# Performance work log

Hardware: AMD Instinct MI355X
Metric: run time of the kernel (lower is better)

## Reference

```python
import jax, jax.numpy as jnp
import numpy as np

B = 2048          # graphs in dense batch
NPG = 64          # nodes per graph (molecules are small)
N = B * NPG       # 131072 total nodes
E = 524288        # directed edges, avg degree 4
D = 275           # dim_inner
L = 5             # layers_mp
NF = 9            # atom categorical features
V = 128           # per-feature vocab
BN_EPS = 1e-5


def setup_inputs() -> dict:
    key = jax.random.key(0)
    ks = jax.random.split(key, 8)
    return {
        "x_atoms": jax.random.randint(ks[0], (N, NF), 0, 119, dtype=jnp.int64),
        "edge_index": jax.random.randint(ks[1], (2, E), 0, N, dtype=jnp.int64),
        "atom_emb": jax.random.normal(ks[2], (NF, V, D), jnp.float32) * 0.1,
        "conv_W": jax.random.normal(ks[3], (L, D, D), jnp.float32) * (1.0 / np.sqrt(D)),
        "conv_b": jnp.zeros((L, D), jnp.float32),
        "bn_gamma": jnp.ones((L, D), jnp.float32),
        "bn_beta": jnp.zeros((L, D), jnp.float32),
        "post_W": jax.random.normal(ks[4], (D, D), jnp.float32) * (1.0 / np.sqrt(D)),
        "post_b": jnp.zeros((D,), jnp.float32),
    }


def reference(x_atoms, edge_index, atom_emb, conv_W, conv_b, bn_gamma, bn_beta, post_W, post_b):
    n = x_atoms.shape[0]
    # AtomEncoder: sum of per-feature embedding lookups -> [N, D]
    h = jax.vmap(lambda tab, idx: tab[idx], in_axes=(0, 1))(atom_emb, x_atoms).sum(0)

    # GCN normalization with self loops (shared across layers since graph is fixed)
    loops = jnp.arange(n, dtype=edge_index.dtype)
    row = jnp.concatenate([edge_index[0], loops])  # source
    col = jnp.concatenate([edge_index[1], loops])  # target (aggregation index)
    deg = jax.ops.segment_sum(jnp.ones_like(row, h.dtype), col, num_segments=n)
    dinv = jnp.where(deg > 0, jax.lax.rsqrt(jnp.maximum(deg, 1e-12)), 0.0)
    norm = dinv[row] * dinv[col]  # [E+N]

    for i in range(L):
        xw = h @ conv_W[i].T                                   # [N, D] linear (no bias yet)
        msg = norm[:, None] * xw[row]                          # gather + edge scaling
        agg = jax.ops.segment_sum(msg, col, num_segments=n) + conv_b[i]
        # BatchNorm1d (training-mode batch stats, biased variance)
        mu = agg.mean(axis=0)
        var = agg.var(axis=0)
        hbn = (agg - mu) * jax.lax.rsqrt(var + BN_EPS) * bn_gamma[i] + bn_beta[i]
        h = jax.nn.relu(hbn)

    # post_mp: single Linear (MLPNoAct, num_layers=1)
    h = h @ post_W.T + post_b

    # graph_preprocess -> dense batch [B, NPG, D], then pairwise dot-product decode
    hd = h.reshape(B, NPG, D)
    logits = jnp.einsum('bnd,bmd->bnm', hd, hd)[..., None]     # [B, NPG, NPG, 1]
    return logits
```

## Files before the change

### kernel.cpp

```cpp
#include <hip/hip_runtime.h>
#include <hip/hip_bf16.h>
#include <cstdint>

#define NN 131072
#define NE 524288
#define DIM 275
#define DP 288
#define NFEAT 9
#define NVOC 128
#define NLAY 5
#define NPG 64
#define NGRAPH 2048
#define BN_EPS 1e-5f
#define BK 32
#define NEPAD (NE + 3 * NN)
#define LDSE 1536

typedef unsigned short u16;
typedef __attribute__((ext_vector_type(8))) short s16x8;
typedef __attribute__((ext_vector_type(4))) float f32x4;

__device__ __forceinline__ float bf2f(u16 u) {
  union { unsigned int i; float f; } x; x.i = ((unsigned int)u) << 16; return x.f;
}
__device__ __forceinline__ u16 f2bf(float f) {
  union { float f; unsigned int i; } x; x.f = f;
  unsigned int r = x.i + 0x7fffu + ((x.i >> 16) & 1u);
  return (u16)(r >> 16);
}
__device__ __forceinline__ void acc4(float* a, uint2 m) {
  a[0] += bf2f((u16)m.x); a[1] += bf2f((u16)(m.x >> 16));
  a[2] += bf2f((u16)m.y); a[3] += bf2f((u16)(m.y >> 16));
}


__global__ void hist_kernel(const int* __restrict__ ei, int* __restrict__ cnt) {
  int e = blockIdx.x * 256 + threadIdx.x;
  if (e < NE) atomicAdd(&cnt[ei[NE + e]], 1);
}

__global__ void pad_dinv_kernel(const int* __restrict__ cnt, int* __restrict__ cnt_pad,
                                float* __restrict__ dinv) {
  int v = blockIdx.x * 256 + threadIdx.x;
  if (v < NN) {
    int c = cnt[v];
    cnt_pad[v] = (c + 3) & ~3;
    dinv[v] = rsqrtf(1.0f + (float)c);
  }
}

__global__ void scan_block_kernel(const int* __restrict__ in, int* __restrict__ out_ex,
                                  int* __restrict__ partials) {
  __shared__ int buf[2][1024];
  int t = threadIdx.x;
  int idx = blockIdx.x * 1024 + t;
  int v = in[idx];
  buf[0][t] = v;
  __syncthreads();
  int cur = 0;
  for (int off = 1; off < 1024; off <<= 1) {
    int x = buf[cur][t];
    if (t >= off) x += buf[cur][t - off];
    buf[cur ^ 1][t] = x;
    __syncthreads();
    cur ^= 1;
  }
  out_ex[idx] = buf[cur][t] - v;
  if (t == 1023) partials[blockIdx.x] = buf[cur][t];
}

__global__ void scan_partials_kernel(int* partials) {
  __shared__ int buf[2][128];
  int t = threadIdx.x;
  int v = partials[t];
  buf[0][t] = v;
  __syncthreads();
  int cur = 0;
  for (int off = 1; off < 128; off <<= 1) {
    int x = buf[cur][t];
    if (t >= off) x += buf[cur][t - off];
    buf[cur ^ 1][t] = x;
    __syncthreads();
    cur ^= 1;
  }
  partials[t] = buf[cur][t] - v;
}

__global__ void add_offsets_kernel(int* __restrict__ indptr, const int* __restrict__ partials,
                                   int* __restrict__ cursor, const int* __restrict__ cnt_pad) {
  int i = blockIdx.x * 256 + threadIdx.x;
  if (i < NN) {
    int v = indptr[i] + partials[i >> 10];
    indptr[i] = v;
    cursor[i] = v;
    if (i == NN - 1) indptr[NN] = v + cnt_pad[NN - 1];
  }
}

__global__ void fill_csr_kernel(const int* __restrict__ ei, int* __restrict__ cursor,
                                int* __restrict__ srcs) {
  int e = blockIdx.x * 256 + threadIdx.x;
  if (e < NE) {
    int c = ei[NE + e];
    int p = atomicAdd(&cursor[c], 1);
    srcs[p] = ei[e];
  }
}

__global__ void pad_fill_kernel(const int* __restrict__ cursor, const int* __restrict__ indptr,
                                int* __restrict__ srcs) {
  int v = blockIdx.x * 256 + threadIdx.x;
  if (v < NN) {
    int pe = indptr[v + 1];
    for (int p = cursor[v]; p < pe; ++p) srcs[p] = NN;
  }
}

__global__ void zrow_kernel(u16* __restrict__ P, u16* __restrict__ Q) {
  int i = threadIdx.x;
  if (i < DP) {
    P[(size_t)NN * DP + i] = 0;
    Q[(size_t)NN * DP + i] = 0;
  }
}

__global__ void wpad_kernel(const float* __restrict__ convW, const float* __restrict__ postW,
                            u16* __restrict__ Wp) {
  int i = blockIdx.x * 256 + threadIdx.x;
  const int total = 6 * 320 * DP;
  if (i >= total) return;
  int k = i % DP;
  int r = i / DP;
  int j = r % 320;
  int m = r / 320;
  float val = 0.f;
  if (j < DIM && k < DIM)
    val = (m < 5) ? convW[((size_t)m * DIM + j) * DIM + k] : postW[(size_t)j * DIM + k];
  Wp[i] = f2bf(val);
}


__global__ void embed_kernel(const int* __restrict__ xa, const float* __restrict__ emb,
                             u16* __restrict__ P) {
  int n = blockIdx.x;
  int idx[NFEAT];
#pragma unroll
  for (int f = 0; f < NFEAT; ++f) idx[f] = xa[n * NFEAT + f];
  for (int d = threadIdx.x; d < DP; d += 128) {
    float s = 0.f;
    if (d < DIM) {
#pragma unroll
      for (int f = 0; f < NFEAT; ++f) s += emb[((size_t)f * NVOC + idx[f]) * DIM + d];
    }
    P[(size_t)n * DP + d] = f2bf(s);
  }
}


__device__ __forceinline__ uint4 xform8s(uint4 r, const float* __restrict__ sc,
                                         const float* __restrict__ sh, int k) {
  union { uint4 u; u16 h[8]; } in, out;
  in.u = r;
#pragma unroll
  for (int j = 0; j < 8; ++j) {
    float x = fmaf(bf2f(in.h[j]), sc[k + j], sh[k + j]);
    out.h[j] = f2bf(fmaxf(x, 0.f));
  }
  return out.u;
}

__launch_bounds__(256)
__global__ void gemm_kernel(const u16* __restrict__ A, const u16* __restrict__ Wp,
                            u16* __restrict__ C,
                            const float* __restrict__ bn_sum, const float* __restrict__ bn_sq,
                            const float* __restrict__ gamma, const float* __restrict__ beta,
                            const float* __restrict__ rowscale, const float* __restrict__ colbias) {
  __shared__ __align__(16) u16 Asl[64 * BK];
  __shared__ __align__(16) u16 Bsl[288 * BK];
  __shared__ float scs[DP], shs[DP];
  const int tid = threadIdx.x, lane = tid & 63, wv = tid >> 6;
  const int wm = wv & 1, wn = wv >> 1;
  const int row0 = blockIdx.x * 64;
  const bool bn = (bn_sum != nullptr);

  for (int d = tid; d < DP; d += 256) {
    float sc = 1.f, sh = 0.f;
    if (bn) {
      if (d < DIM) {
        const float invN = 1.0f / (float)NN;
        float mu = bn_sum[d] * invN;
        float var = bn_sq[d] * invN - mu * mu;
        float rstd = rsqrtf(var + BN_EPS);
        sc = gamma[d] * rstd;
        sh = fmaf(-mu, sc, beta[d]);
      } else {
        sc = 0.f; sh = 0.f;
      }
    }
    scs[d] = sc; shs[d] = sh;
  }

  const int srow = tid >> 2, schk = tid & 3;
  const int swz = ((schk ^ (srow & 3) ^ ((srow >> 2) & 3)) << 3);
  const int awoff = srow * BK + swz;
  const u16* ag = A + (size_t)(row0 + srow) * DP + schk * 8;
  const u16* bg = Wp + (size_t)srow * DP + schk * 8;
  const bool st4 = (tid < 128);

  const int fr = lane & 15, fs = lane >> 4;
  int aoff[2], boff[9];
#pragma unroll
  for (int i = 0; i < 2; ++i) {
    int r = wm * 32 + i * 16 + fr;
    aoff[i] = r * BK + ((fs ^ (r & 3) ^ ((r >> 2) & 3)) << 3);
  }
#pragma unroll
  for (int j = 0; j < 9; ++j) {
    int r = wn * 144 + j * 16 + fr;
    boff[j] = r * BK + ((fs ^ (r & 3) ^ ((r >> 2) & 3)) << 3);
  }

  uint4 ra = *(const uint4*)(ag);
  uint4 rb0 = *(const uint4*)(bg);
  uint4 rb1 = *(const uint4*)(bg + (size_t)64 * DP);
  uint4 rb2 = *(const uint4*)(bg + (size_t)128 * DP);
  uint4 rb3 = *(const uint4*)(bg + (size_t)192 * DP);
  uint4 rb4;
  if (st4) rb4 = *(const uint4*)(bg + (size_t)256 * DP);
  __syncthreads();
  if (bn) ra = xform8s(ra, scs, shs, schk * 8);
  *(uint4*)&Asl[awoff] = ra;
  *(uint4*)&Bsl[awoff] = rb0;
  *(uint4*)&Bsl[awoff + 64 * BK] = rb1;
  *(uint4*)&Bsl[awoff + 128 * BK] = rb2;
  *(uint4*)&Bsl[awoff + 192 * BK] = rb3;
  if (st4) *(uint4*)&Bsl[awoff + 256 * BK] = rb4;
  __syncthreads();

  f32x4 acc0[9], acc1[9];
#pragma unroll
  for (int j = 0; j < 9; ++j) {
    acc0[j] = (f32x4){0.f, 0.f, 0.f, 0.f};
    acc1[j] = (f32x4){0.f, 0.f, 0.f, 0.f};
  }

#pragma unroll 1
  for (int s = 0; s < 9; ++s) {
    const bool more = (s < 8);
    uint4 na, nb0, nb1, nb2, nb3, nb4;
    if (more) {
      int k = (s + 1) * BK;
      na = *(const uint4*)(ag + k);
      nb0 = *(const uint4*)(bg + k);
      nb1 = *(const uint4*)(bg + (size_t)64 * DP + k);
      nb2 = *(const uint4*)(bg + (size_t)128 * DP + k);
      nb3 = *(const uint4*)(bg + (size_t)192 * DP + k);
      if (st4) nb4 = *(const uint4*)(bg + (size_t)256 * DP + k);
    }
    s16x8 af0 = *(const s16x8*)&Asl[aoff[0]];
    s16x8 af1 = *(const s16x8*)&Asl[aoff[1]];
#pragma unroll
    for (int j = 0; j < 9; ++j) {
      s16x8 bf = *(const s16x8*)&Bsl[boff[j]];
      acc0[j] = __builtin_amdgcn_mfma_f32_16x16x32_bf16(af0, bf, acc0[j], 0, 0, 0);
      acc1[j] = __builtin_amdgcn_mfma_f32_16x16x32_bf16(af1, bf, acc1[j], 0, 0, 0);
    }
    __syncthreads();
    if (more) {
      if (bn) na = xform8s(na, scs, shs, (s + 1) * BK + schk * 8);
      *(uint4*)&Asl[awoff] = na;
      *(uint4*)&Bsl[awoff] = nb0;
      *(uint4*)&Bsl[awoff + 64 * BK] = nb1;
      *(uint4*)&Bsl[awoff + 128 * BK] = nb2;
      *(uint4*)&Bsl[awoff + 192 * BK] = nb3;
      if (st4) *(uint4*)&Bsl[awoff + 256 * BK] = nb4;
      __syncthreads();
    }
  }

#pragma unroll
  for (int i = 0; i < 2; ++i) {
    int gr0 = row0 + wm * 32 + i * 16 + fs * 4;
    float rs[4];
#pragma unroll
    for (int r = 0; r < 4; ++r) rs[r] = rowscale ? rowscale[gr0 + r] : 1.f;
#pragma unroll
    for (int j = 0; j < 9; ++j) {
      f32x4 av = i ? acc1[j] : acc0[j];
      int gc = wn * 144 + j * 16 + fr;
      float cb = (colbias && gc < DIM) ? colbias[gc] : 0.f;
#pragma unroll
      for (int r = 0; r < 4; ++r) {
        u16 o = (gc < DIM) ? f2bf(fmaf(av[r], rs[r], cb)) : (u16)0;
        C[(size_t)(gr0 + r) * DP + gc] = o;
      }
    }
  }
}


__launch_bounds__(256)
__global__ void spmm_kernel(const u16* __restrict__ X, u16* __restrict__ Y,
                            const int* __restrict__ indptr, const int* __restrict__ srcs,
                            const float* __restrict__ dinv, const float* __restrict__ bias,
                            float* __restrict__ bn_sum, float* __restrict__ bn_sq) {
  __shared__ float ls[DP], lq[DP];
  __shared__ int sptr[65];
  __shared__ int sidx[LDSE];
  int tid = threadIdx.x;
  for (int i = tid; i < DP; i += 256) { ls[i] = 0.f; lq[i] = 0.f; }
  int vb = blockIdx.x * 64;
  if (tid < 65) sptr[tid] = indptr[vb + tid];
  __syncthreads();
  int ebase = sptr[0];
  int ecnt = sptr[64] - ebase;
  const int* ip;
  if (ecnt <= LDSE) {
    for (int i = tid; i < ecnt; i += 256) sidx[i] = srcs[ebase + i];
    ip = sidx;
  } else {
    ip = srcs + ebase;
  }
  __syncthreads();

  int lane = tid & 63, wv = tid >> 6;
  int c0 = lane << 2;
  int c1 = 256 + (lane << 2);
  bool tl = lane < 8;
  float bia[4], bib[4];
#pragma unroll
  for (int j = 0; j < 4; ++j) bia[j] = bias[c0 + j];
#pragma unroll
  for (int j = 0; j < 4; ++j) bib[j] = (tl && c1 + j < DIM) ? bias[c1 + j] : 0.f;
  float s0[4] = {}, q0[4] = {}, s1[4] = {}, q1[4] = {};

  for (int g = 0; g < 8; ++g) {
    int nA = wv * 16 + g;
    int nB = nA + 8;
    int ebA = sptr[nA] - ebase, neA = sptr[nA + 1] - sptr[nA];
    int ebB = sptr[nB] - ebase, neB = sptr[nB + 1] - sptr[nB];
    int nemax = neA > neB ? neA : neB;
    const u16* xA = X + (size_t)(vb + nA) * DP;
    const u16* xB = X + (size_t)(vb + nB) * DP;
    uint2 mA = *(const uint2*)(xA + c0);
    uint2 mB = *(const uint2*)(xB + c0);
    uint2 tA, tB;
    if (tl) { tA = *(const uint2*)(xA + c1); tB = *(const uint2*)(xB + c1); }
    float A0[4] = {}, B0[4] = {}, A1[4] = {}, B1[4] = {};
    acc4(A0, mA); acc4(B0, mB);
    if (tl) { acc4(A1, tA); acc4(B1, tB); }

    for (int e = 0; e < nemax; e += 4) {
      bool aA = e < neA, aB = e < neB;
      int oA = aA ? ebA + e : 0;
      int oB = aB ? ebB + e : 0;
      int ia[4], ib[4];
#pragma unroll
      for (int j = 0; j < 4; ++j) {
        int va = ip[oA + j], vbx = ip[oB + j];
        ia[j] = aA ? va : NN;
        ib[j] = aB ? vbx : NN;
      }
      const u16* pa[4]; const u16* pb[4];
#pragma unroll
      for (int j = 0; j < 4; ++j) {
        pa[j] = X + (size_t)ia[j] * DP;
        pb[j] = X + (size_t)ib[j] * DP;
      }
      uint2 ma[4], mb[4];
#pragma unroll
      for (int j = 0; j < 4; ++j) ma[j] = *(const uint2*)(pa[j] + c0);
#pragma unroll
      for (int j = 0; j < 4; ++j) mb[j] = *(const uint2*)(pb[j] + c0);
      uint2 ta[4], tb[4];
      if (tl) {
#pragma unroll
        for (int j = 0; j < 4; ++j) ta[j] = *(const uint2*)(pa[j] + c1);
#pragma unroll
        for (int j = 0; j < 4; ++j) tb[j] = *(const uint2*)(pb[j] + c1);
      }
#pragma unroll
      for (int j = 0; j < 4; ++j) { acc4(A0, ma[j]); acc4(B0, mb[j]); }
      if (tl) {
#pragma unroll
        for (int j = 0; j < 4; ++j) { acc4(A1, ta[j]); acc4(B1, tb[j]); }
      }
    }

    float dvA = dinv[vb + nA], dvB = dinv[vb + nB];
    u16* yA = Y + (size_t)(vb + nA) * DP;
    u16* yB = Y + (size_t)(vb + nB) * DP;
    float ya[4], yb[4];
#pragma unroll
    for (int j = 0; j < 4; ++j) {
      ya[j] = fmaf(dvA, A0[j], bia[j]);
      s0[j] += ya[j]; q0[j] += ya[j] * ya[j];
      yb[j] = fmaf(dvB, B0[j], bia[j]);
      s0[j] += yb[j]; q0[j] += yb[j] * yb[j];
    }
    uint2 wa, wb;
    wa.x = (unsigned)f2bf(ya[0]) | ((unsigned)f2bf(ya[1]) << 16);
    wa.y = (unsigned)f2bf(ya[2]) | ((unsigned)f2bf(ya[3]) << 16);
    wb.x = (unsigned)f2bf(yb[0]) | ((unsigned)f2bf(yb[1]) << 16);
    wb.y = (unsigned)f2bf(yb[2]) | ((unsigned)f2bf(yb[3]) << 16);
    *(uint2*)(yA + c0) = wa;
    *(uint2*)(yB + c0) = wb;
    if (tl) {
      float za[4], zb[4];
#pragma unroll
      for (int j = 0; j < 4; ++j) {
        za[j] = fmaf(dvA, A1[j], bib[j]);
        s1[j] += za[j]; q1[j] += za[j] * za[j];
        zb[j] = fmaf(dvB, B1[j], bib[j]);
        s1[j] += zb[j]; q1[j] += zb[j] * zb[j];
      }
      uint2 ua, ub;
      ua.x = (unsigned)f2bf(za[0]) | ((unsigned)f2bf(za[1]) << 16);
      ua.y = (unsigned)f2bf(za[2]) | ((unsigned)f2bf(za[3]) << 16);
      ub.x = (unsigned)f2bf(zb[0]) | ((unsigned)f2bf(zb[1]) << 16);
      ub.y = (unsigned)f2bf(zb[2]) | ((unsigned)f2bf(zb[3]) << 16);
      *(uint2*)(yA + c1) = ua;
      *(uint2*)(yB + c1) = ub;
    }
  }

#pragma unroll
  for (int j = 0; j < 4; ++j) { atomicAdd(&ls[c0 + j], s0[j]); atomicAdd(&lq[c0 + j], q0[j]); }
  if (tl) {
#pragma unroll
    for (int j = 0; j < 4; ++j) { atomicAdd(&ls[c1 + j], s1[j]); atomicAdd(&lq[c1 + j], q1[j]); }
  }
  __syncthreads();
  for (int i = tid; i < DP; i += 256) {
    atomicAdd(&bn_sum[i], ls[i]);
    atomicAdd(&bn_sq[i], lq[i]);
  }
}


__launch_bounds__(256)
__global__ void decode_kernel(const u16* __restrict__ H, float* __restrict__ out) {
  __shared__ __align__(16) u16 tile[4][2][NPG * BK];
  int tid = threadIdx.x, lane = tid & 63, wv = tid >> 6;
  int g = blockIdx.x * 4 + wv;
  const u16* Hg = H + (size_t)g * NPG * DP;
  const int ssl = lane & 3;
  int soff[4];
  const u16* sg[4];
#pragma unroll
  for (int i = 0; i < 4; ++i) {
    int r = (lane >> 2) + i * 16;
    soff[i] = r * BK + ((ssl ^ (r & 3) ^ ((r >> 2) & 3)) << 3);
    sg[i] = Hg + (size_t)r * DP + ssl * 8;
  }
  const int fr = lane & 15, fs = lane >> 4;
  const int fswz = ((fs ^ (fr & 3) ^ ((fr >> 2) & 3)) << 3);
  int foff[4];
#pragma unroll
  for (int i = 0; i < 4; ++i) foff[i] = (i * 16 + fr) * BK + fswz;

  u16* t0 = tile[wv][0];
  u16* t1 = tile[wv][1];
  uint4 rg[4];
#pragma unroll
  for (int i = 0; i < 4; ++i) rg[i] = *(const uint4*)(sg[i]);
#pragma unroll
  for (int i = 0; i < 4; ++i) *(uint4*)&t0[soff[i]] = rg[i];

  f32x4 acc[4][4];
#pragma unroll
  for (int i = 0; i < 4; ++i)
#pragma unroll
    for (int j = 0; j < 4; ++j) acc[i][j] = (f32x4){0.f, 0.f, 0.f, 0.f};

  for (int s = 0; s < DP / BK; ++s) {
    u16* cur = (s & 1) ? t1 : t0;
    u16* nxt = (s & 1) ? t0 : t1;
    const bool more = (s < DP / BK - 1);
    if (more) {
#pragma unroll
      for (int i = 0; i < 4; ++i) rg[i] = *(const uint4*)(sg[i] + (s + 1) * BK);
    }
    s16x8 af[4];
#pragma unroll
    for (int i = 0; i < 4; ++i) af[i] = *(const s16x8*)&cur[foff[i]];
#pragma unroll
    for (int i = 0; i < 4; ++i)
#pragma unroll
      for (int j = 0; j < 4; ++j)
        acc[i][j] = __builtin_amdgcn_mfma_f32_16x16x32_bf16(af[i], af[j], acc[i][j], 0, 0, 0);
    if (more) {
#pragma unroll
      for (int i = 0; i < 4; ++i) *(uint4*)&nxt[soff[i]] = rg[i];
    }
  }
  float* og = out + (size_t)g * NPG * NPG;
#pragma unroll
  for (int i = 0; i < 4; ++i) {
    int m0 = i * 16 + fs * 4;
#pragma unroll
    for (int j = 0; j < 4; ++j) {
      int n = j * 16 + fr;
#pragma unroll
      for (int r = 0; r < 4; ++r) og[(m0 + r) * NPG + n] = acc[i][j][r];
    }
  }
}


extern "C" void kernel_launch(void* const* d_in, const int* in_sizes, int n_in,
                              void* d_out, int out_size, void* d_ws, size_t ws_size,
                              hipStream_t stream) {
  const int* xa = (const int*)d_in[0];
  const int* ei = (const int*)d_in[1];
  const float* emb = (const float*)d_in[2];
  const float* convW = (const float*)d_in[3];
  const float* convB = (const float*)d_in[4];
  const float* gamma = (const float*)d_in[5];
  const float* beta = (const float*)d_in[6];
  const float* postW = (const float*)d_in[7];
  const float* postB = (const float*)d_in[8];
  float* out = (float*)d_out;

  char* w = (char*)d_ws;
  u16* P = (u16*)w;          w += (size_t)(NN + 1) * DP * sizeof(u16);
  u16* Q = (u16*)w;          w += (size_t)(NN + 1) * DP * sizeof(u16);
  u16* Wp = (u16*)w;         w += (size_t)6 * 320 * DP * sizeof(u16);
  float* dinv = (float*)w;   w += (size_t)NN * sizeof(float);
  int* cnt = (int*)w;        w += (size_t)NN * sizeof(int);
  int* cnt_pad = (int*)w;    w += (size_t)NN * sizeof(int);
  int* indptr = (int*)w;     w += (size_t)(NN + 64) * sizeof(int);
  int* cursor = (int*)w;     w += (size_t)NN * sizeof(int);
  int* srcs = (int*)w;       w += (size_t)NEPAD * sizeof(int);
  int* partials = (int*)w;   w += 256 * sizeof(int);
  float* bnstats = (float*)w; w += (size_t)NLAY * 2 * DP * sizeof(float);

  size_t need = (size_t)(w - (char*)d_ws);
  if (ws_size < need) return;

  hipMemsetAsync(cnt, 0, (size_t)NN * sizeof(int), stream);
  hipMemsetAsync(bnstats, 0, (size_t)NLAY * 2 * DP * sizeof(float), stream);
  hist_kernel<<<NE / 256, 256, 0, stream>>>(ei, cnt);
  pad_dinv_kernel<<<NN / 256, 256, 0, stream>>>(cnt, cnt_pad, dinv);
  scan_block_kernel<<<NN / 1024, 1024, 0, stream>>>(cnt_pad, indptr, partials);
  scan_partials_kernel<<<1, 128, 0, stream>>>(partials);
  add_offsets_kernel<<<NN / 256, 256, 0, stream>>>(indptr, partials, cursor, cnt_pad);
  fill_csr_kernel<<<NE / 256, 256, 0, stream>>>(ei, cursor, srcs);
  pad_fill_kernel<<<NN / 256, 256, 0, stream>>>(cursor, indptr, srcs);
  wpad_kernel<<<(6 * 320 * DP + 255) / 256, 256, 0, stream>>>(convW, postW, Wp);
  embed_kernel<<<NN, 128, 0, stream>>>(xa, emb, P);
  zrow_kernel<<<1, 288, 0, stream>>>(P, Q);

  for (int l = 0; l < NLAY; ++l) {
    const float* bs = l ? bnstats + (size_t)(l - 1) * 2 * DP : nullptr;
    gemm_kernel<<<NN / 64, 256, 0, stream>>>(
        P, Wp + (size_t)l * 320 * DP, Q,
        bs, bs ? bs + DP : nullptr,
        l ? gamma + (size_t)(l - 1) * DIM : nullptr,
        l ? beta + (size_t)(l - 1) * DIM : nullptr,
        dinv, nullptr);
    spmm_kernel<<<NN / 64, 256, 0, stream>>>(Q, P, indptr, srcs, dinv,
                                             convB + (size_t)l * DIM,
                                             bnstats + (size_t)l * 2 * DP,
                                             bnstats + (size_t)l * 2 * DP + DP);
  }

  const float* bs5 = bnstats + (size_t)4 * 2 * DP;
  gemm_kernel<<<NN / 64, 256, 0, stream>>>(
      P, Wp + (size_t)5 * 320 * DP, Q, bs5, bs5 + DP,
      gamma + (size_t)4 * DIM, beta + (size_t)4 * DIM, nullptr, postB);

  decode_kernel<<<NGRAPH / 4, 256, 0, stream>>>(Q, out);
}
```

Before: 1.030 ms.

## Double-buffer GEMM LDS with direct global-to-LDS weight loads; rebalance SpMM tail lanes

The weight matrix is now stored pre-swizzled so the GEMM can copy B tiles straight from global memory into LDS with global_load_lds. A and B tiles are double-buffered, which drops one barrier per k-step and overlaps the next tile's load with the MFMAs. In the SpMM, the 19-column tail of each node pair is spread over 16 lanes (8 per node) instead of 8 lanes each handling both nodes, and edge indices are read from LDS as int4 vectors. The cost is double the GEMM LDS footprint, which may lower occupancy, and int4 index reads that depend on 16-byte-aligned offsets in the padded edge list.

```diff
diff --git a/kernel.cpp b/kernel.cpp
--- a/kernel.cpp
+++ b/kernel.cpp
@@ -20,6 +20,10 @@
 typedef __attribute__((ext_vector_type(8))) short s16x8;
 typedef __attribute__((ext_vector_type(4))) float f32x4;
 
+#define GLL16(g, l) __builtin_amdgcn_global_load_lds( \
+    (const __attribute__((address_space(1))) unsigned int*)(g), \
+    (__attribute__((address_space(3))) unsigned int*)(l), 16, 0, 0)
+
 __device__ __forceinline__ float bf2f(u16 u) {
   union { unsigned int i; float f; } x; x.i = ((unsigned int)u) << 16; return x.f;
 }
@@ -136,7 +140,9 @@
   float val = 0.f;
   if (j < DIM && k < DIM)
     val = (m < 5) ? convW[((size_t)m * DIM + j) * DIM + k] : postW[(size_t)j * DIM + k];
-  Wp[i] = f2bf(val);
+  int s = (j & 3) ^ ((j >> 2) & 3);
+  int kout = (k & ~24) | (((((k >> 3) & 3)) ^ s) << 3);
+  Wp[(size_t)r * DP + kout] = f2bf(val);
 }
 
 
@@ -170,13 +176,13 @@
 }
 
 __launch_bounds__(256)
-__global__ void gemm_kernel(const u16* __restrict__ A, const u16* __restrict__ Wp,
+__global__ void gemm_kernel(const u16* __restrict__ A, const u16* __restrict__ Wq,
                             u16* __restrict__ C,
                             const float* __restrict__ bn_sum, const float* __restrict__ bn_sq,
                             const float* __restrict__ gamma, const float* __restrict__ beta,
                             const float* __restrict__ rowscale, const float* __restrict__ colbias) {
-  __shared__ __align__(16) u16 Asl[64 * BK];
-  __shared__ __align__(16) u16 Bsl[288 * BK];
+  __shared__ __align__(16) u16 Asl[2][64 * BK];
+  __shared__ __align__(16) u16 Bsl[2][288 * BK];
   __shared__ float scs[DP], shs[DP];
   const int tid = threadIdx.x, lane = tid & 63, wv = tid >> 6;
   const int wm = wv & 1, wn = wv >> 1;
@@ -204,8 +210,7 @@
   const int swz = ((schk ^ (srow & 3) ^ ((srow >> 2) & 3)) << 3);
   const int awoff = srow * BK + swz;
   const u16* ag = A + (size_t)(row0 + srow) * DP + schk * 8;
-  const u16* bg = Wp + (size_t)srow * DP + schk * 8;
-  const bool st4 = (tid < 128);
+  const int grow = lane >> 2, gchk = (lane & 3) * 8;
 
   const int fr = lane & 15, fs = lane >> 4;
   int aoff[2], boff[9];
@@ -220,21 +225,12 @@
     boff[j] = r * BK + ((fs ^ (r & 3) ^ ((r >> 2) & 3)) << 3);
   }
 
+  for (int i = wv; i < 18; i += 4)
+    GLL16(Wq + (size_t)(i * 16 + grow) * DP + gchk, &Bsl[0][i * 512]);
   uint4 ra = *(const uint4*)(ag);
-  uint4 rb0 = *(const uint4*)(bg);
-  uint4 rb1 = *(const uint4*)(bg + (size_t)64 * DP);
-  uint4 rb2 = *(const uint4*)(bg + (size_t)128 * DP);
-  uint4 rb3 = *(const uint4*)(bg + (size_t)192 * DP);
-  uint4 rb4;
-  if (st4) rb4 = *(const uint4*)(bg + (size_t)256 * DP);
   __syncthreads();
   if (bn) ra = xform8s(ra, scs, shs, schk * 8);
-  *(uint4*)&Asl[awoff] = ra;
-  *(uint4*)&Bsl[awoff] = rb0;
-  *(uint4*)&Bsl[awoff + 64 * BK] = rb1;
-  *(uint4*)&Bsl[awoff + 128 * BK] = rb2;
-  *(uint4*)&Bsl[awoff + 192 * BK] = rb3;
-  if (st4) *(uint4*)&Bsl[awoff + 256 * BK] = rb4;
+  *(uint4*)&Asl[0][awoff] = ra;
   __syncthreads();
 
   f32x4 acc0[9], acc1[9];
@@ -246,36 +242,28 @@
 
 #pragma unroll 1
   for (int s = 0; s < 9; ++s) {
+    const int cur = s & 1;
     const bool more = (s < 8);
-    uint4 na, nb0, nb1, nb2, nb3, nb4;
+    uint4 na;
     if (more) {
       int k = (s + 1) * BK;
+      for (int i = wv; i < 18; i += 4)
+        GLL16(Wq + (size_t)(i * 16 + grow) * DP + k + gchk, &Bsl[cur ^ 1][i * 512]);
       na = *(const uint4*)(ag + k);
-      nb0 = *(const uint4*)(bg + k);
-      nb1 = *(const uint4*)(bg + (size_t)64 * DP + k);
-      nb2 = *(const uint4*)(bg + (size_t)128 * DP + k);
-      nb3 = *(const uint4*)(bg + (size_t)192 * DP + k);
-      if (st4) nb4 = *(const uint4*)(bg + (size_t)256 * DP + k);
-    }
-    s16x8 af0 = *(const s16x8*)&Asl[aoff[0]];
-    s16x8 af1 = *(const s16x8*)&Asl[aoff[1]];
+    }
+    s16x8 af0 = *(const s16x8*)&Asl[cur][aoff[0]];
+    s16x8 af1 = *(const s16x8*)&Asl[cur][aoff[1]];
 #pragma unroll
     for (int j = 0; j < 9; ++j) {
-      s16x8 bf = *(const s16x8*)&Bsl[boff[j]];
+      s16x8 bf = *(const s16x8*)&Bsl[cur][boff[j]];
       acc0[j] = __builtin_amdgcn_mfma_f32_16x16x32_bf16(af0, bf, acc0[j], 0, 0, 0);
       acc1[j] = __builtin_amdgcn_mfma_f32_16x16x32_bf16(af1, bf, acc1[j], 0, 0, 0);
     }
-    __syncthreads();
     if (more) {
       if (bn) na = xform8s(na, scs, shs, (s + 1) * BK + schk * 8);
-      *(uint4*)&Asl[awoff] = na;
-      *(uint4*)&Bsl[awoff] = nb0;
-      *(uint4*)&Bsl[awoff + 64 * BK] = nb1;
-      *(uint4*)&Bsl[awoff + 128 * BK] = nb2;
-      *(uint4*)&Bsl[awoff + 192 * BK] = nb3;
-      if (st4) *(uint4*)&Bsl[awoff + 256 * BK] = nb4;
-      __syncthreads();
-    }
+      *(uint4*)&Asl[cur ^ 1][awoff] = na;
+    }
+    __syncthreads();
   }
 
 #pragma unroll
@@ -306,7 +294,7 @@
                             float* __restrict__ bn_sum, float* __restrict__ bn_sq) {
   __shared__ float ls[DP], lq[DP];
   __shared__ int sptr[65];
-  __shared__ int sidx[LDSE];
+  __shared__ __align__(16) int sidx[LDSE];
   int tid = threadIdx.x;
   for (int i = tid; i < DP; i += 256) { ls[i] = 0.f; lq[i] = 0.f; }
   int vb = blockIdx.x * 64;
@@ -325,8 +313,10 @@
 
   int lane = tid & 63, wv = tid >> 6;
   int c0 = lane << 2;
-  int c1 = 256 + (lane << 2);
-  bool tl = lane < 8;
+  int lane2 = lane & 7;
+  int c1 = 256 + (lane2 << 2);
+  bool tl = lane < 16;
+  bool loA = lane < 8;
   float bia[4], bib[4];
 #pragma unroll
   for (int j = 0; j < 4; ++j) bia[j] = bias[c0 + j];
@@ -344,23 +334,23 @@
     const u16* xB = X + (size_t)(vb + nB) * DP;
     uint2 mA = *(const uint2*)(xA + c0);
     uint2 mB = *(const uint2*)(xB + c0);
-    uint2 tA, tB;
-    if (tl) { tA = *(const uint2*)(xA + c1); tB = *(const uint2*)(xB + c1); }
-    float A0[4] = {}, B0[4] = {}, A1[4] = {}, B1[4] = {};
+    uint2 tS;
+    if (tl) tS = *(const uint2*)((loA ? xA : xB) + c1);
+    float A0[4] = {}, B0[4] = {}, C1[4] = {};
     acc4(A0, mA); acc4(B0, mB);
-    if (tl) { acc4(A1, tA); acc4(B1, tB); }
+    if (tl) acc4(C1, tS);
 
     for (int e = 0; e < nemax; e += 4) {
       bool aA = e < neA, aB = e < neB;
       int oA = aA ? ebA + e : 0;
       int oB = aB ? ebB + e : 0;
+      int4 i4a = *(const int4*)(ip + oA);
+      int4 i4b = *(const int4*)(ip + oB);
       int ia[4], ib[4];
-#pragma unroll
-      for (int j = 0; j < 4; ++j) {
-        int va = ip[oA + j], vbx = ip[oB + j];
-        ia[j] = aA ? va : NN;
-        ib[j] = aB ? vbx : NN;
-      }
+      ia[0] = aA ? i4a.x : NN; ia[1] = aA ? i4a.y : NN;
+      ia[2] = aA ? i4a.z : NN; ia[3] = aA ? i4a.w : NN;
+      ib[0] = aB ? i4b.x : NN; ib[1] = aB ? i4b.y : NN;
+      ib[2] = aB ? i4b.z : NN; ib[3] = aB ? i4b.w : NN;
       const u16* pa[4]; const u16* pb[4];
 #pragma unroll
       for (int j = 0; j < 4; ++j) {
@@ -372,18 +362,16 @@
       for (int j = 0; j < 4; ++j) ma[j] = *(const uint2*)(pa[j] + c0);
 #pragma unroll
       for (int j = 0; j < 4; ++j) mb[j] = *(const uint2*)(pb[j] + c0);
-      uint2 ta[4], tb[4];
+      uint2 tc[4];
       if (tl) {
 #pragma unroll
-        for (int j = 0; j < 4; ++j) ta[j] = *(const uint2*)(pa[j] + c1);
-#pragma unroll
-        for (int j = 0; j < 4; ++j) tb[j] = *(const uint2*)(pb[j] + c1);
+        for (int j = 0; j < 4; ++j) tc[j] = *(const uint2*)((loA ? pa[j] : pb[j]) + c1);
       }
 #pragma unroll
       for (int j = 0; j < 4; ++j) { acc4(A0, ma[j]); acc4(B0, mb[j]); }
       if (tl) {
 #pragma unroll
-        for (int j = 0; j < 4; ++j) { acc4(A1, ta[j]); acc4(B1, tb[j]); }
+        for (int j = 0; j < 4; ++j) acc4(C1, tc[j]);
       }
     }
 
@@ -406,21 +394,18 @@
     *(uint2*)(yA + c0) = wa;
     *(uint2*)(yB + c0) = wb;
     if (tl) {
-      float za[4], zb[4];
+      float dvS = loA ? dvA : dvB;
+      u16* yS = loA ? yA : yB;
+      float z[4];
 #pragma unroll
       for (int j = 0; j < 4; ++j) {
-        za[j] = fmaf(dvA, A1[j], bib[j]);
-        s1[j] += za[j]; q1[j] += za[j] * za[j];
-        zb[j] = fmaf(dvB, B1[j], bib[j]);
-        s1[j] += zb[j]; q1[j] += zb[j] * zb[j];
+        z[j] = fmaf(dvS, C1[j], bib[j]);
+        s1[j] += z[j]; q1[j] += z[j] * z[j];
       }
-      uint2 ua, ub;
-      ua.x = (unsigned)f2bf(za[0]) | ((unsigned)f2bf(za[1]) << 16);
-      ua.y = (unsigned)f2bf(za[2]) | ((unsigned)f2bf(za[3]) << 16);
-      ub.x = (unsigned)f2bf(zb[0]) | ((unsigned)f2bf(zb[1]) << 16);
-      ub.y = (unsigned)f2bf(zb[2]) | ((unsigned)f2bf(zb[3]) << 16);
-      *(uint2*)(yA + c1) = ua;
-      *(uint2*)(yB + c1) = ub;
+      uint2 w2;
+      w2.x = (unsigned)f2bf(z[0]) | ((unsigned)f2bf(z[1]) << 16);
+      w2.y = (unsigned)f2bf(z[2]) | ((unsigned)f2bf(z[3]) << 16);
+      *(uint2*)(yS + c1) = w2;
     }
   }
 
```

After: 996.6 us. 3.2% less time.
